# Kernel tuning notes

Hardware: AMD Instinct MI355X
Metric: run time of the kernel (lower is better)

## Reference

```python
import jax, jax.numpy as jnp
import numpy as np
import math

H, D, DFF = 12, 768, 3072
DH = D // H  # 64
B, T = 4, 2048
EPS = 1e-5


def setup_inputs() -> dict:
    key = jax.random.key(0)
    ks = jax.random.split(key, 12)
    randw = lambda k, *d: jax.random.normal(k, d, jnp.float32) / math.sqrt(d[-1])
    return {
        "X": jax.random.normal(ks[0], (B, T, D), jnp.float32),
        "w_q": randw(ks[1], H, DH, D),
        "w_k": randw(ks[2], H, DH, D),
        "w_v": randw(ks[3], H, DH, D),
        "w_o": randw(ks[4], DH * H, D),
        "W1": jax.random.normal(ks[5], (DFF, D), jnp.float32) * 0.02,
        "b1": jnp.zeros((DFF,), jnp.float32),
        "W2": jax.random.normal(ks[6], (D, DFF), jnp.float32) * 0.02,
        "b2": jnp.zeros((D,), jnp.float32),
        "g1": jnp.ones((D,), jnp.float32),
        "be1": jnp.zeros((D,), jnp.float32),
        "g2": jnp.ones((D,), jnp.float32),
        "be2": jnp.zeros((D,), jnp.float32),
    }


def layernorm(x, g, b):
    mu = jnp.mean(x, axis=-1, keepdims=True)
    var = jnp.var(x, axis=-1, keepdims=True)
    return (x - mu) * jax.lax.rsqrt(var + EPS) * g + b


def attention(x, w_q, w_k, w_v, w_o):
    # x: [n,t,c]
    q = jnp.einsum('ntc,hdc->nhtd', x, w_q)
    k = jnp.einsum('ntc,hdc->nhtd', x, w_k)
    v = jnp.einsum('ntc,hdc->nhtd', x, w_v)
    a = jnp.einsum('nhtd,nhsd->nhts', q, k) / math.sqrt(q.shape[3])
    t, s = a.shape[2], a.shape[3]
    forbidden = jnp.arange(t)[:, None] < jnp.arange(s)[None, :]
    a = jnp.where(forbidden, -jnp.inf, a)
    a = jax.nn.softmax(a, axis=3)
    y = jnp.einsum('nhts,nhsd->nthd', a, v).reshape(x.shape[0], t, -1)
    return y @ w_o


def reference(X, w_q, w_k, w_v, w_o, W1, b1, W2, b2, g1, be1, g2, be2):
    X = X + attention(layernorm(X, g1, be1), w_q, w_k, w_v, w_o)
    h = jax.nn.relu(layernorm(X, g2, be2) @ W1.T + b1)
    return X + h @ W2.T + b2
```

## Files before the change

kernel.cpp:

```cpp
#include <hip/hip_runtime.h>
#include <stdint.h>

#define B_   4
#define T_   2048
#define D_   768
#define H_   12
#define DH_  64
#define DFF_ 3072
#define NTOK_ (B_*T_)
#define QKVN_ (3*D_)

typedef unsigned short u16;
typedef unsigned int u32;
typedef __bf16 bf16x8 __attribute__((ext_vector_type(8)));
typedef float  f32x4  __attribute__((ext_vector_type(4)));

__device__ __forceinline__ u16 f2bf(float f) {
  union { float f; unsigned u; } v; v.f = f;
  return (u16)((v.u + 0x7fffu + ((v.u >> 16) & 1u)) >> 16);
}

__device__ __forceinline__ u32 pack_bf2(float a, float b) {
  union { float f; u32 u; } ua, ub; ua.f = a; ub.f = b;
  return ((ua.u + 0x8000u) >> 16) | ((ub.u + 0x8000u) & 0xFFFF0000u);
}

__device__ __forceinline__ float fast_exp2(float x) {
#if __has_builtin(__builtin_amdgcn_exp2f)
  return __builtin_amdgcn_exp2f(x);
#else
  return exp2f(x);
#endif
}

__device__ __forceinline__ float fast_rcp(float x) {
#if __has_builtin(__builtin_amdgcn_rcpf)
  return __builtin_amdgcn_rcpf(x);
#else
  return 1.0f / x;
#endif
}

__device__ __forceinline__ void gload_lds16(const void* g, void* l) {
  __builtin_amdgcn_global_load_lds(
      (__attribute__((address_space(1))) unsigned int*)(void*)g,
      (__attribute__((address_space(3))) unsigned int*)l, 16, 0, 0);
}

template<bool BIAS, bool RELU, bool RES, bool BF16OUT, bool QSCALE, int BN,
         bool VTRANS>
__global__ __launch_bounds__(256) void gemm_bt(
    const u16* __restrict__ A, const u16* __restrict__ Bw,
    const float* __restrict__ bias, const float* __restrict__ res,
    void* __restrict__ outp, u16* __restrict__ vtp, int M, int N, int K)
{
  constexpr int NI = BN / 32;
  __shared__ u16 lA[2 * 128 * 32];
  __shared__ u16 lB[2 * BN * 32];
  const int tid  = threadIdx.x;
  const int lane = tid & 63;
  const int wave = tid >> 6;
  const int quad = lane >> 4;
  const int l15  = lane & 15;
  const int mBase = blockIdx.x * 128;
  const int nBase = blockIdx.y * BN;
  const int wm = (wave >> 1) * 64;
  const int wn = (wave & 1) * (BN / 2);

  const f32x4 fz = {0.f, 0.f, 0.f, 0.f};
  f32x4 acc[4][NI];
#pragma unroll
  for (int i = 0; i < 4; i++)
#pragma unroll
    for (int j = 0; j < NI; j++) acc[i][j] = fz;

  const int c0 = tid, c1 = tid + 256;
  const u16* gA0 = A  + (size_t)(mBase + (c0 >> 2)) * K + (c0 & 3) * 8;
  const u16* gA1 = A  + (size_t)(mBase + (c1 >> 2)) * K + (c1 & 3) * 8;
  const u16* gB0 = Bw + (size_t)(nBase + (c0 >> 2)) * K + (c0 & 3) * 8;
  const u16* gB1 = (BN == 128)
      ? Bw + (size_t)(nBase + (c1 >> 2)) * K + (c1 & 3) * 8 : nullptr;
  u16* lA0 = lA + c0 * 8; u16* lA1 = lA + c1 * 8;
  u16* lB0 = lB + c0 * 8;
  u16* lB1 = (BN == 128) ? lB + c1 * 8 : nullptr;

  for (int kt = 0; kt < K; kt += 64) {
    gload_lds16(gA0 + kt,      lA0);
    gload_lds16(gA1 + kt,      lA1);
    gload_lds16(gA0 + kt + 32, lA0 + 128 * 32);
    gload_lds16(gA1 + kt + 32, lA1 + 128 * 32);
    gload_lds16(gB0 + kt,      lB0);
    gload_lds16(gB0 + kt + 32, lB0 + BN * 32);
    if (BN == 128) {
      gload_lds16(gB1 + kt,      lB1);
      gload_lds16(gB1 + kt + 32, lB1 + BN * 32);
    }
    __syncthreads();
#pragma unroll
    for (int hf = 0; hf < 2; hf++) {
      const u16* lAh = lA + hf * (128 * 32);
      const u16* lBh = lB + hf * (BN * 32);
      bf16x8 af[4], bfr[NI];
#pragma unroll
      for (int mi = 0; mi < 4; mi++)
        af[mi] = *(const bf16x8*)(lAh + (wm + mi * 16 + l15) * 32 + quad * 8);
#pragma unroll
      for (int ni = 0; ni < NI; ni++)
        bfr[ni] = *(const bf16x8*)(lBh + (wn + ni * 16 + l15) * 32 + quad * 8);
#pragma unroll
      for (int mi = 0; mi < 4; mi++)
#pragma unroll
        for (int ni = 0; ni < NI; ni++)
          acc[mi][ni] = __builtin_amdgcn_mfma_f32_16x16x32_bf16(
              af[mi], bfr[ni], acc[mi][ni], 0, 0, 0);
    }
    __syncthreads();
  }

#pragma unroll
  for (int mi = 0; mi < 4; mi++) {
#pragma unroll
    for (int ni = 0; ni < NI; ni++) {
      const int col = nBase + wn + ni * 16 + l15;
      if (VTRANS && col >= 2 * D_) {
        const int n  = col - 2 * D_;
        const int hh = n >> 6, dd = n & 63;
        const int row0 = mBase + wm + mi * 16 + quad * 4;
        const int bb = row0 >> 11, tt = row0 & (T_ - 1);
        const int tperm = (tt & ~31) + 8 * quad + 4 * (mi & 1);
        ushort4 pk;
        pk.x = f2bf(acc[mi][ni][0]); pk.y = f2bf(acc[mi][ni][1]);
        pk.z = f2bf(acc[mi][ni][2]); pk.w = f2bf(acc[mi][ni][3]);
        *(ushort4*)(vtp + ((size_t)((bb * H_ + hh) * DH_ + dd)) * T_ + tperm) = pk;
        continue;
      }
      float bv = 0.f;
      if (BIAS) bv = bias[col];
#pragma unroll
      for (int r = 0; r < 4; r++) {
        const int row = mBase + wm + mi * 16 + quad * 4 + r;
        float v = acc[mi][ni][r];
        if (BIAS) v += bv;
        if (RELU) v = fmaxf(v, 0.f);
        if (RES)  v += res[(size_t)row * N + col];
        if (QSCALE && col < D_) v *= 0.180336880f;
        if (BF16OUT) ((u16*)outp)[(size_t)row * N + col] = f2bf(v);
        else        ((float*)outp)[(size_t)row * N + col] = v;
      }
    }
  }
}

__device__ __forceinline__ void attn_round(
    const u16* __restrict__ lKc, const u16* __restrict__ lVc,
    int s0, int qw0, int quad, int l15,
    int kc0, int kc1,
    const bf16x8& q0, const bf16x8& q1,
    f32x4 (&o)[4], float& ls)
{
  const f32x4 fz = {0.f, 0.f, 0.f, 0.f};
  f32x4 s[4];
#pragma unroll
  for (int ni = 0; ni < 4; ni++) {
    const int rb = (ni * 16 + l15) * 64;
    const bf16x8 k0 = *(const bf16x8*)(lKc + rb + kc0);
    const bf16x8 k1 = *(const bf16x8*)(lKc + rb + kc1);
    f32x4 t = fz;
    t = __builtin_amdgcn_mfma_f32_16x16x32_bf16(k0, q0, t, 0, 0, 0);
    t = __builtin_amdgcn_mfma_f32_16x16x32_bf16(k1, q1, t, 0, 0, 0);
    s[ni] = t;
  }

  const bool nm = (s0 + 63 > qw0);
  const int qidx = qw0 + l15;
  u32 pk[8];
#pragma unroll
  for (int ni = 0; ni < 4; ni++) {
    const int sbase = s0 + ni * 16 + quad * 4;
    float p[4];
#pragma unroll
    for (int r = 0; r < 4; r++) {
      float v = fast_exp2(s[ni][r]);
      if (nm && (sbase + r > qidx)) v = 0.f;
      p[r] = v;
      ls += v;
    }
    pk[ni * 2]     = pack_bf2(p[0], p[1]);
    pk[ni * 2 + 1] = pack_bf2(p[2], p[3]);
  }
  union { u32 u[8]; bf16x8 v[2]; } P;
#pragma unroll
  for (int i = 0; i < 8; i++) P.u[i] = pk[i];

#pragma unroll
  for (int dt = 0; dt < 4; dt++) {
    const int rb = (dt * 16 + l15) * 64;
    const bf16x8 v0 = *(const bf16x8*)(lVc + rb + kc0);
    const bf16x8 v1 = *(const bf16x8*)(lVc + rb + kc1);
    o[dt] = __builtin_amdgcn_mfma_f32_16x16x32_bf16(v0, P.v[0], o[dt], 0, 0, 0);
    o[dt] = __builtin_amdgcn_mfma_f32_16x16x32_bf16(v1, P.v[1], o[dt], 0, 0, 0);
  }
}

__global__ __launch_bounds__(256) void attn_kernel(
    const u16* __restrict__ qkv, const u16* __restrict__ vt, u16* __restrict__ Y)
{
  __shared__ u16 lK[2][64 * 64];
  __shared__ u16 lV[2][64 * 64];
  const int tid  = threadIdx.x;
  const int lane = tid & 63;
  const int wave = tid >> 6;
  const int quad = lane >> 4;
  const int l15  = lane & 15;
  const int pi = (int)blockIdx.x;
  const int h  = blockIdx.y;
  const int b  = blockIdx.z;
  const int tH = 31 - pi, tL = pi;
  const int njsH = tH + 1;
  const int total = njsH + tL + 1;
  const int qwH = tH * 64 + wave * 16;
  const int qwL = tL * 64 + wave * 16;

  const int sw  = l15 & 7;
  const int kc0 = (quad ^ sw) * 8;
  const int kc1 = ((4 + quad) ^ sw) * 8;

  bf16x8 qH0, qH1, qL0, qL1;
  {
    const u16* qp = qkv + (size_t)(b * T_ + qwH + l15) * QKVN_ + h * DH_ + quad * 8;
    qH0 = *(const bf16x8*)(qp);
    qH1 = *(const bf16x8*)(qp + 32);
    const u16* qp2 = qkv + (size_t)(b * T_ + qwL + l15) * QKVN_ + h * DH_ + quad * 8;
    qL0 = *(const bf16x8*)(qp2);
    qL1 = *(const bf16x8*)(qp2 + 32);
  }

  const f32x4 fz = {0.f, 0.f, 0.f, 0.f};
  f32x4 oH[4], oL[4];
#pragma unroll
  for (int i = 0; i < 4; i++) { oH[i] = fz; oL[i] = fz; }
  float lsH = 0.f, lsL = 0.f;

  const int c0 = tid, c1 = tid + 256;
  const int r0 = c0 >> 3, j0 = (c0 & 7) ^ (r0 & 7);
  const int r1 = c1 >> 3, j1 = (c1 & 7) ^ (r1 & 7);
  const u16* gK0 = qkv + (size_t)(b * T_ + r0) * QKVN_ + D_ + h * DH_ + j0 * 8;
  const u16* gK1 = qkv + (size_t)(b * T_ + r1) * QKVN_ + D_ + h * DH_ + j1 * 8;
  const u16* gV0 = vt + (size_t)((b * H_ + h) * DH_ + r0) * T_ + j0 * 8;
  const u16* gV1 = vt + (size_t)((b * H_ + h) * DH_ + r1) * T_ + j1 * 8;

  gload_lds16(gK0, lK[0] + c0 * 8);
  gload_lds16(gK1, lK[0] + c1 * 8);
  gload_lds16(gV0, lV[0] + c0 * 8);
  gload_lds16(gV1, lV[0] + c1 * 8);

  for (int i = 0; i < total; i++) {
    const int cur = i & 1;
    __syncthreads();

    if (i + 1 < total) {
      const int sn = (i + 1 < njsH) ? (i + 1) : (i + 1 - njsH);
      const size_t s1 = (size_t)sn * 64;
      const int nb = cur ^ 1;
      gload_lds16(gK0 + s1 * QKVN_, lK[nb] + c0 * 8);
      gload_lds16(gK1 + s1 * QKVN_, lK[nb] + c1 * 8);
      gload_lds16(gV0 + s1,         lV[nb] + c0 * 8);
      gload_lds16(gV1 + s1,         lV[nb] + c1 * 8);
    }

    const u16* lKc = lK[cur];
    const u16* lVc = lV[cur];
    if (i < njsH) {
      attn_round(lKc, lVc, i * 64, qwH, quad, l15, kc0, kc1,
                 qH0, qH1, oH, lsH);
    } else {
      attn_round(lKc, lVc, (i - njsH) * 64, qwL, quad, l15, kc0, kc1,
                 qL0, qL1, oL, lsL);
    }
  }

  lsH += __shfl_xor(lsH, 16); lsH += __shfl_xor(lsH, 32);
  lsL += __shfl_xor(lsL, 16); lsL += __shfl_xor(lsL, 32);
  const float rlH = fast_rcp(lsH);
  const float rlL = fast_rcp(lsL);

#pragma unroll
  for (int dt = 0; dt < 4; dt++) {
    const int dbase = h * DH_ + dt * 16 + quad * 4;
    ushort4 pa, pb;
    pa.x = f2bf(oH[dt][0] * rlH); pa.y = f2bf(oH[dt][1] * rlH);
    pa.z = f2bf(oH[dt][2] * rlH); pa.w = f2bf(oH[dt][3] * rlH);
    pb.x = f2bf(oL[dt][0] * rlL); pb.y = f2bf(oL[dt][1] * rlL);
    pb.z = f2bf(oL[dt][2] * rlL); pb.w = f2bf(oL[dt][3] * rlL);
    *(ushort4*)(Y + (size_t)(b * T_ + qwH + l15) * D_ + dbase) = pa;
    *(ushort4*)(Y + (size_t)(b * T_ + qwL + l15) * D_ + dbase) = pb;
  }
}

__device__ __forceinline__ void ln_row(
    const float* __restrict__ X, const float* __restrict__ g,
    const float* __restrict__ be, u16* __restrict__ out, int row)
{
  const float* x = X + (size_t)row * D_;
  const int t = threadIdx.x;
  const float v0 = x[t], v1 = x[t + 256], v2 = x[t + 512];
  float s = v0 + v1 + v2;
  float sq = v0 * v0 + v1 * v1 + v2 * v2;
#pragma unroll
  for (int off = 1; off < 64; off <<= 1) {
    s  += __shfl_xor(s, off);
    sq += __shfl_xor(sq, off);
  }
  __shared__ float ws_[4], wq_[4];
  const int wv = t >> 6, lane = t & 63;
  if (lane == 0) { ws_[wv] = s; wq_[wv] = sq; }
  __syncthreads();
  s  = ws_[0] + ws_[1] + ws_[2] + ws_[3];
  sq = wq_[0] + wq_[1] + wq_[2] + wq_[3];
  const float mean = s * (1.f / 768.f);
  const float var  = sq * (1.f / 768.f) - mean * mean;
  const float rstd = rsqrtf(var + 1e-5f);
  u16* o = out + (size_t)row * D_;
  int c = t;
  o[c] = f2bf((v0 - mean) * rstd * g[c] + be[c]); c += 256;
  o[c] = f2bf((v1 - mean) * rstd * g[c] + be[c]); c += 256;
  o[c] = f2bf((v2 - mean) * rstd * g[c] + be[c]);
}

__global__ __launch_bounds__(256) void ln_kernel(
    const float* __restrict__ X, const float* __restrict__ g,
    const float* __restrict__ be, u16* __restrict__ out)
{
  ln_row(X, g, be, out, blockIdx.x);
}

__global__ __launch_bounds__(256) void prep_kernel(
    const float* __restrict__ X, const float* __restrict__ g1,
    const float* __restrict__ be1, u16* __restrict__ xln,
    const float* __restrict__ w_q, const float* __restrict__ w_k,
    const float* __restrict__ w_v, const float* __restrict__ W1,
    const float* __restrict__ W2, const float* __restrict__ w_o,
    u16* __restrict__ wqkv, u16* __restrict__ W1b,
    u16* __restrict__ W2b, u16* __restrict__ woT)
{
  if (blockIdx.x < NTOK_) {
    ln_row(X, g1, be1, xln, blockIdx.x);
    return;
  }
  const int id = blockIdx.x - NTOK_;
  if (id < 144) {
    __shared__ float tile[64][65];
    const int bx = id % 12, by = id / 12;
    const int rr0 = by * 64, cc0 = bx * 64;
    for (int idx = threadIdx.x; idx < 4096; idx += 256) {
      const int i = idx >> 6, j = idx & 63;
      tile[i][j] = w_o[(size_t)(rr0 + i) * D_ + cc0 + j];
    }
    __syncthreads();
    for (int idx = threadIdx.x; idx < 4096; idx += 256) {
      const int i = idx >> 6, j = idx & 63;
      woT[(size_t)(cc0 + i) * D_ + rr0 + j] = f2bf(tile[j][i]);
    }
  } else {
    const int WQN = H_ * DH_ * D_;
    const int i = (id - 144) * 256 + threadIdx.x;
    if (i < 3 * WQN) {
      const float* src = (i < WQN) ? w_q : (i < 2 * WQN ? w_k : w_v);
      const int off = (i < WQN) ? i : (i < 2 * WQN ? i - WQN : i - 2 * WQN);
      wqkv[i] = f2bf(src[off]);
    } else if (i < 3 * WQN + DFF_ * D_) {
      const int off = i - 3 * WQN;
      W1b[off] = f2bf(W1[off]);
    } else {
      const int off = i - 3 * WQN - DFF_ * D_;
      W2b[off] = f2bf(W2[off]);
    }
  }
}

extern "C" void kernel_launch(void* const* d_in, const int* in_sizes, int n_in,
                              void* d_out, int out_size, void* d_ws, size_t ws_size,
                              hipStream_t stream) {
  const float* X   = (const float*)d_in[0];
  const float* w_q = (const float*)d_in[1];
  const float* w_k = (const float*)d_in[2];
  const float* w_v = (const float*)d_in[3];
  const float* w_o = (const float*)d_in[4];
  const float* W1  = (const float*)d_in[5];
  const float* b1  = (const float*)d_in[6];
  const float* W2  = (const float*)d_in[7];
  const float* b2  = (const float*)d_in[8];
  const float* g1  = (const float*)d_in[9];
  const float* be1 = (const float*)d_in[10];
  const float* g2  = (const float*)d_in[11];
  const float* be2 = (const float*)d_in[12];
  float* out = (float*)d_out;

  char* ws = (char*)d_ws;
  u16*   qkv  = (u16*)(ws + 0);
  u16*   vt   = (u16*)(ws + 37748736);
  u16*   hbuf = (u16*)(ws + 0);
  u16*   xln  = (u16*)(ws + 50331648);
  u16*   Ybuf = (u16*)(ws + 62914560);
  float* X1   = (float*)(ws + 75497472);
  u16*   wqkv = (u16*)(ws + 100663296);
  u16*   woT  = (u16*)(ws + 104202240);
  u16*   W1b  = (u16*)(ws + 105381888);
  u16*   W2b  = (u16*)(ws + 110100480);

  prep_kernel<<<NTOK_ + 25488, 256, 0, stream>>>(
      X, g1, be1, xln, w_q, w_k, w_v, W1, W2, w_o, wqkv, W1b, W2b, woT);

  gemm_bt<false, false, false, true, true, 128, true>
      <<<dim3(64, 18), 256, 0, stream>>>(
      xln, wqkv, nullptr, nullptr, qkv, vt, NTOK_, QKVN_, D_);

  attn_kernel<<<dim3(16, 12, 4), 256, 0, stream>>>(qkv, vt, Ybuf);

  gemm_bt<false, false, true, false, false, 64, false>
      <<<dim3(64, 12), 256, 0, stream>>>(
      Ybuf, woT, nullptr, X, X1, nullptr, NTOK_, D_, D_);

  ln_kernel<<<NTOK_, 256, 0, stream>>>(X1, g2, be2, xln);

  gemm_bt<true, true, false, true, false, 128, false>
      <<<dim3(64, 24), 256, 0, stream>>>(
      xln, W1b, b1, nullptr, hbuf, nullptr, NTOK_, DFF_, D_);

  gemm_bt<true, false, true, false, false, 64, false>
      <<<dim3(64, 12), 256, 0, stream>>>(
      hbuf, W2b, b2, X1, out, nullptr, NTOK_, D_, DFF_);
}
```

Measured before the change: 365.2 us.

## Software-pipeline attention: overlap QK^T of next tile with PV of previous tile

Splits the attention round into QK matmul, exp/pack, and PV matmul stages. The PV product for tile i-1 is now issued alongside the QK product for tile i, so MFMA work can overlap with the exp/mask ALU work. V gets a third LDS buffer to hold the lagging tile, and s_setprio raises wave priority around the MFMA section. This adds register pressure (live scores and P) and more LDS use, which could lower occupancy.

```diff
diff --git a/kernel.cpp b/kernel.cpp
--- a/kernel.cpp
+++ b/kernel.cpp
@@ -151,15 +151,11 @@
   }
 }
 
-__device__ __forceinline__ void attn_round(
-    const u16* __restrict__ lKc, const u16* __restrict__ lVc,
-    int s0, int qw0, int quad, int l15,
-    int kc0, int kc1,
-    const bf16x8& q0, const bf16x8& q1,
-    f32x4 (&o)[4], float& ls)
+__device__ __forceinline__ void qk_mm(
+    const u16* __restrict__ lKc, int kc0, int kc1, int l15,
+    const bf16x8& q0, const bf16x8& q1, f32x4 (&s)[4])
 {
   const f32x4 fz = {0.f, 0.f, 0.f, 0.f};
-  f32x4 s[4];
 #pragma unroll
   for (int ni = 0; ni < 4; ni++) {
     const int rb = (ni * 16 + l15) * 64;
@@ -170,28 +166,15 @@
     t = __builtin_amdgcn_mfma_f32_16x16x32_bf16(k1, q1, t, 0, 0, 0);
     s[ni] = t;
   }
-
-  const bool nm = (s0 + 63 > qw0);
-  const int qidx = qw0 + l15;
-  u32 pk[8];
-#pragma unroll
-  for (int ni = 0; ni < 4; ni++) {
-    const int sbase = s0 + ni * 16 + quad * 4;
-    float p[4];
-#pragma unroll
-    for (int r = 0; r < 4; r++) {
-      float v = fast_exp2(s[ni][r]);
-      if (nm && (sbase + r > qidx)) v = 0.f;
-      p[r] = v;
-      ls += v;
-    }
-    pk[ni * 2]     = pack_bf2(p[0], p[1]);
-    pk[ni * 2 + 1] = pack_bf2(p[2], p[3]);
-  }
+}
+
+__device__ __forceinline__ void pv_mm(
+    const u16* __restrict__ lVc, int kc0, int kc1, int l15,
+    const u32 (&Pp)[8], f32x4 (&o)[4])
+{
   union { u32 u[8]; bf16x8 v[2]; } P;
 #pragma unroll
-  for (int i = 0; i < 8; i++) P.u[i] = pk[i];
-
+  for (int i = 0; i < 8; i++) P.u[i] = Pp[i];
 #pragma unroll
   for (int dt = 0; dt < 4; dt++) {
     const int rb = (dt * 16 + l15) * 64;
@@ -202,11 +185,31 @@
   }
 }
 
+__device__ __forceinline__ void exp_pack(
+    const f32x4 (&s)[4], int s0, int qidx, bool nm, int quad,
+    u32 (&Pp)[8], float& ls)
+{
+#pragma unroll
+  for (int ni = 0; ni < 4; ni++) {
+    const int sbase = s0 + ni * 16 + quad * 4;
+    float p[4];
+#pragma unroll
+    for (int r = 0; r < 4; r++) {
+      float v = fast_exp2(s[ni][r]);
+      if (nm && (sbase + r > qidx)) v = 0.f;
+      p[r] = v;
+      ls += v;
+    }
+    Pp[ni * 2]     = pack_bf2(p[0], p[1]);
+    Pp[ni * 2 + 1] = pack_bf2(p[2], p[3]);
+  }
+}
+
 __global__ __launch_bounds__(256) void attn_kernel(
     const u16* __restrict__ qkv, const u16* __restrict__ vt, u16* __restrict__ Y)
 {
   __shared__ u16 lK[2][64 * 64];
-  __shared__ u16 lV[2][64 * 64];
+  __shared__ u16 lV[3][64 * 64];
   const int tid  = threadIdx.x;
   const int lane = tid & 63;
   const int wave = tid >> 6;
@@ -217,7 +220,7 @@
   const int b  = blockIdx.z;
   const int tH = 31 - pi, tL = pi;
   const int njsH = tH + 1;
-  const int total = njsH + tL + 1;
+  const int njsL = tL + 1;
   const int qwH = tH * 64 + wave * 16;
   const int qwL = tL * 64 + wave * 16;
 
@@ -240,6 +243,8 @@
 #pragma unroll
   for (int i = 0; i < 4; i++) { oH[i] = fz; oL[i] = fz; }
   float lsH = 0.f, lsL = 0.f;
+  u32 Pp[8];
+  f32x4 sS[4];
 
   const int c0 = tid, c1 = tid + 256;
   const int r0 = c0 >> 3, j0 = (c0 & 7) ^ (r0 & 7);
@@ -254,30 +259,52 @@
   gload_lds16(gV0, lV[0] + c0 * 8);
   gload_lds16(gV1, lV[0] + c1 * 8);
 
-  for (int i = 0; i < total; i++) {
-    const int cur = i & 1;
+  int kcur = 0;
+  int va = 2, vb = 0, vc = 1;
+
+  for (int i = 0; i < njsH; i++) {
     __syncthreads();
-
-    if (i + 1 < total) {
-      const int sn = (i + 1 < njsH) ? (i + 1) : (i + 1 - njsH);
+    {
+      const int sn = (i + 1 < njsH) ? (i + 1) : 0;
       const size_t s1 = (size_t)sn * 64;
-      const int nb = cur ^ 1;
-      gload_lds16(gK0 + s1 * QKVN_, lK[nb] + c0 * 8);
-      gload_lds16(gK1 + s1 * QKVN_, lK[nb] + c1 * 8);
-      gload_lds16(gV0 + s1,         lV[nb] + c0 * 8);
-      gload_lds16(gV1 + s1,         lV[nb] + c1 * 8);
-    }
-
-    const u16* lKc = lK[cur];
-    const u16* lVc = lV[cur];
-    if (i < njsH) {
-      attn_round(lKc, lVc, i * 64, qwH, quad, l15, kc0, kc1,
-                 qH0, qH1, oH, lsH);
-    } else {
-      attn_round(lKc, lVc, (i - njsH) * 64, qwL, quad, l15, kc0, kc1,
-                 qL0, qL1, oL, lsL);
-    }
-  }
+      u16* lKn = lK[kcur ^ 1] ;
+      u16* lVn = lV[vc];
+      gload_lds16(gK0 + s1 * QKVN_, lKn + c0 * 8);
+      gload_lds16(gK1 + s1 * QKVN_, lKn + c1 * 8);
+      gload_lds16(gV0 + s1,         lVn + c0 * 8);
+      gload_lds16(gV1 + s1,         lVn + c1 * 8);
+    }
+    const u16* lKc = lK[kcur];
+    __builtin_amdgcn_s_setprio(1);
+    qk_mm(lKc, kc0, kc1, l15, qH0, qH1, sS);
+    if (i > 0) pv_mm(&lV[va][0], kc0, kc1, l15, Pp, oH);
+    __builtin_amdgcn_s_setprio(0);
+    exp_pack(sS, i * 64, qwH + l15, i == njsH - 1, quad, Pp, lsH);
+    kcur ^= 1;
+    const int t = va; va = vb; vb = vc; vc = t;
+  }
+  for (int j = 0; j < njsL; j++) {
+    __syncthreads();
+    if (j + 1 < njsL) {
+      const size_t s1 = (size_t)(j + 1) * 64;
+      u16* lKn = lK[kcur ^ 1];
+      u16* lVn = lV[vc];
+      gload_lds16(gK0 + s1 * QKVN_, lKn + c0 * 8);
+      gload_lds16(gK1 + s1 * QKVN_, lKn + c1 * 8);
+      gload_lds16(gV0 + s1,         lVn + c0 * 8);
+      gload_lds16(gV1 + s1,         lVn + c1 * 8);
+    }
+    const u16* lKc = lK[kcur];
+    __builtin_amdgcn_s_setprio(1);
+    qk_mm(lKc, kc0, kc1, l15, qL0, qL1, sS);
+    if (j == 0) pv_mm(&lV[va][0], kc0, kc1, l15, Pp, oH);
+    else        pv_mm(&lV[va][0], kc0, kc1, l15, Pp, oL);
+    __builtin_amdgcn_s_setprio(0);
+    exp_pack(sS, j * 64, qwL + l15, j == njsL - 1, quad, Pp, lsL);
+    kcur ^= 1;
+    const int t = va; va = vb; vb = vc; vc = t;
+  }
+  pv_mm(&lV[va][0], kc0, kc1, l15, Pp, oL);
 
   lsH += __shfl_xor(lsH, 16); lsH += __shfl_xor(lsH, 32);
   lsL += __shfl_xor(lsL, 16); lsL += __shfl_xor(lsL, 32);
```

Result: slower. 379.1 us (+3.8%).
